# Kernel tuning notes

Hardware: AMD Instinct MI355X
Metric: run time of the kernel (lower is better)

The kernel has to match this reference:

```python
import jax, jax.numpy as jnp
import numpy as np

N_USER, N_ITEM, N_ENT = 60000, 30000, 15000
E_UI, E_IE = 1_000_000, 300_000
DIM, FACTOR_K, DIM_K, ITERS = 50, 2, 25, 4
INDEX = [(0, 1), (1, 0)] + [(1, j) for j in range(2, 8)]
I_LIST = [[0], [1, 2, 3, 4, 5, 6, 7]]


def _l2n(x):
    # F.normalize(p=2, dim=2), eps=1e-12
    return x / jnp.clip(jnp.linalg.norm(x, axis=2, keepdims=True), 1e-12)


def _forward(edges, embs_in, Wtk, at, W, q_rela):
    n_types = len(embs_in)
    # fac(): project each node type into factor_k subspaces [k, n, dim_k]
    embs = [_l2n(jax.nn.leaky_relu(jnp.einsum('nd,kde->kne', embs_in[i], Wtk[i]), 0.2))
            for i in range(n_types)]
    rows = [embs[a].shape[1] for (a, b) in INDEX]
    # r_rela init: uniform over factors, never fed back (as in the source)
    r_node = [jnp.full((FACTOR_K, rows[e]), 1.0 / FACTOR_K, dtype=embs[0].dtype)
              for e in range(len(INDEX))]

    def rela_update(edge, new_emb, old_emb, a, r_n, n_rows, q_r):
        u, col = edge[0], edge[1]
        # edge gather + attention score per factor: [k, E]
        ui = jnp.concatenate([new_emb[:, u], old_emb[:, col]], axis=2)  # [k,E,2*dk]
        e_ts_k = jax.nn.relu(jnp.einsum('ked,kd->ke', ui, a))
        vals = jnp.sum(e_ts_k * r_n[:, u], axis=0)  # [E]
        # sparse row-wise softmax (torch.sparse.softmax dim=1)
        m = jax.ops.segment_max(vals, u, num_segments=n_rows)
        ex = jnp.exp(vals - m[u])
        attn = ex / jax.ops.segment_sum(ex, u, num_segments=n_rows)[u]
        # sparse mm per factor: scatter attn-weighted neighbor features
        msg = attn[None, :, None] * old_emb[:, col]  # [k,E,dk]
        z = jax.vmap(lambda mk: jax.ops.segment_sum(mk, u, num_segments=n_rows))(msg)
        z = jnp.einsum('kne,ef->knf', jax.nn.leaky_relu(z, 0.2), W)
        r = jax.nn.softmax(jnp.einsum('kne,e->kn', jnp.tanh(z), q_r), axis=0)
        return r, z

    # note: in the source all_new_emb aliases all_ego_emb (same list), so updates persist
    for _ in range(ITERS):
        rl, el = [], []
        for e in range(len(INDEX)):
            a_i, b_i = INDEX[e]
            r, z = rela_update(edges[e], embs[a_i], embs[b_i], at[e], r_node[e], rows[e], q_rela[e])
            rl.append(r)
            el.append(z)
        for i in range(2):
            ego = embs[i]
            for j in I_LIST[i]:
                ego = ego + el[j] * rl[j][:, :, None]
            embs[i] = _l2n(ego)

    def flat(e):  # torch.cat(list(e), dim=1): [k,n,d] -> [n, k*d]
        k, n, d = e.shape
        return jnp.transpose(e, (1, 0, 2)).reshape(n, k * d)

    return jnp.concatenate([flat(embs[0]), flat(embs[1])], axis=0)


def setup_inputs() -> dict:
    key = jax.random.key(0)
    ks = jax.random.split(key, 40)
    inp = {}

    def edges(k1, k2, E, nr, nc):
        r = jax.random.randint(k1, (E,), 0, nr)
        c = jax.random.randint(k2, (E,), 0, nc)
        return jnp.stack([r, c]).astype(jnp.int32)

    inp['edge0'] = edges(ks[0], ks[1], E_UI, N_USER, N_ITEM)
    inp['edge1'] = edges(ks[2], ks[3], E_UI, N_ITEM, N_USER)
    for e in range(2, 8):
        inp[f'edge{e}'] = edges(ks[2 * e], ks[2 * e + 1], E_IE, N_ITEM, N_ENT)
    sizes = [N_USER, N_ITEM] + [N_ENT] * 6
    for i, n in enumerate(sizes):
        inp[f'emb{i}'] = jax.random.normal(ks[16 + i], (n, DIM), jnp.float32) * 0.1
    inp['Wtk'] = jax.random.normal(ks[30], (8, FACTOR_K, DIM, DIM_K), jnp.float32) * (2.0 / (DIM + DIM_K)) ** 0.5
    inp['at'] = jax.random.normal(ks[31], (8, FACTOR_K, 2 * DIM_K), jnp.float32) * 0.1
    inp['W'] = jax.random.normal(ks[32], (DIM_K, DIM_K), jnp.float32) * 0.2
    inp['q_rela'] = jax.random.normal(ks[33], (8, DIM_K), jnp.float32) * 0.2
    return inp


def reference(edge0, edge1, edge2, edge3, edge4, edge5, edge6, edge7,
              emb0, emb1, emb2, emb3, emb4, emb5, emb6, emb7,
              Wtk, at, W, q_rela):
    edges = [edge0, edge1, edge2, edge3, edge4, edge5, edge6, edge7]
    embs_in = [emb0, emb1, emb2, emb3, emb4, emb5, emb6, emb7]
    return _forward(edges, embs_in, Wtk, at, W, q_rela)
```

## Files before the change

### kernel.cpp

```cpp
#include <hip/hip_runtime.h>
#include <math.h>


#define KF 2
#define DK 25
#define DD 50
#define PS 52
#define ITERS 4
#define WPB 4

static __device__ __forceinline__ float leakyf(float x) { return x > 0.f ? x : 0.2f * x; }

static __device__ __forceinline__ float2 score_row50(const float* p, const float* a) {
    float s0 = 0.f, s1 = 0.f;
    #pragma unroll
    for (int f = 0; f < DK; ++f) {
        s0 = fmaf(p[f],      a[f],      s0);
        s1 = fmaf(p[DK + f], a[50 + f], s1);
    }
    return make_float2(s0, s1);
}
static __device__ __forceinline__ float2 score_col50(const float* p, const float* a) {
    float s0 = 0.f, s1 = 0.f;
    #pragma unroll
    for (int f = 0; f < DK; ++f) {
        s0 = fmaf(p[f],      a[25 + f], s0);
        s1 = fmaf(p[DK + f], a[75 + f], s1);
    }
    return make_float2(s0, s1);
}

struct FacArgs { const float* emb[8]; float* P[8]; const float* Wtk; int base[9]; };

__global__ void fac_kernel(FacArgs A) {
    int g = blockIdx.x * blockDim.x + threadIdx.x;
    if (g >= A.base[8]) return;
    int ty = 0;
    while (g >= A.base[ty + 1]) ++ty;
    int node = g - A.base[ty];
    const float* er = A.emb[ty] + (size_t)node * DD;
    const float* Wt = A.Wtk + (size_t)ty * KF * DD * DK;
    float x[DD];
    #pragma unroll
    for (int d = 0; d < DD; ++d) x[d] = er[d];
    float out[DD];
    #pragma unroll
    for (int k = 0; k < KF; ++k) {
        const float* Wk = Wt + k * DD * DK;
        float nrm = 0.f;
        for (int f = 0; f < DK; ++f) {
            float acc = 0.f;
            for (int d = 0; d < DD; ++d) acc = fmaf(x[d], Wk[d * DK + f], acc);
            acc = leakyf(acc);
            out[k * DK + f] = acc;
            nrm = fmaf(acc, acc, nrm);
        }
        float inv = 1.f / fmaxf(sqrtf(nrm), 1e-12f);
        for (int f = 0; f < DK; ++f) out[k * DK + f] *= inv;
    }
    float* Pr = A.P[ty] + (size_t)node * PS;
    #pragma unroll
    for (int j = 0; j < DD; ++j) Pr[j] = out[j];
    Pr[50] = 0.f; Pr[51] = 0.f;
}

struct EdgeArgs {
    const int* rows[8]; const int* cols[8];
    int* cnt;
    unsigned short* colind;
    int ebase[9];
    int rowbase[8];
};

__global__ void hist_kernel(EdgeArgs A) {
    int g = blockIdx.x * blockDim.x + threadIdx.x;
    if (g >= A.ebase[8]) return;
    int rel = 0;
    while (g >= A.ebase[rel + 1]) ++rel;
    int e = g - A.ebase[rel];
    atomicAdd(&A.cnt[A.rowbase[rel] + A.rows[rel][e]], 1);
}

__global__ __launch_bounds__(1024) void scan_part_kernel(int* a, int n, int* bsum) {
    __shared__ int lds[1024];
    int tid = threadIdx.x;
    int i = blockIdx.x * 1024 + tid;
    int v = (i < n) ? a[i] : 0;
    lds[tid] = v;
    __syncthreads();
    int x = v;
    for (int off = 1; off < 1024; off <<= 1) {
        int y = (tid >= off) ? lds[tid - off] : 0;
        __syncthreads();
        x += y;
        lds[tid] = x;
        __syncthreads();
    }
    if (i < n) a[i] = x - v;
    if (tid == 1023) bsum[blockIdx.x] = x;
}

__global__ __launch_bounds__(1024) void scan_bsum_kernel(int* bsum, int nb) {
    __shared__ int lds[1024];
    int tid = threadIdx.x;
    int v = (tid < nb) ? bsum[tid] : 0;
    lds[tid] = v;
    __syncthreads();
    int x = v;
    for (int off = 1; off < 1024; off <<= 1) {
        int y = (tid >= off) ? lds[tid - off] : 0;
        __syncthreads();
        x += y;
        lds[tid] = x;
        __syncthreads();
    }
    if (tid < nb) bsum[tid] = x - v;
}

__global__ __launch_bounds__(1024) void add_off_kernel(int* a, int n, const int* bsum) {
    int i = blockIdx.x * 1024 + threadIdx.x;
    if (i < n) a[i] += bsum[blockIdx.x];
}

__global__ void scatter_kernel(EdgeArgs A) {
    int g = blockIdx.x * blockDim.x + threadIdx.x;
    if (g >= A.ebase[8]) return;
    int rel = 0;
    while (g >= A.ebase[rel + 1]) ++rel;
    int e = g - A.ebase[rel];
    int p = atomicAdd(&A.cnt[A.rowbase[rel] + A.rows[rel][e]], 1);
    A.colind[p] = (unsigned short)A.cols[rel][e];
}

struct SbArgs { const float* Pb[6]; const float* at[6]; float2* sb[6]; int base[7]; };

__global__ void sb_kernel(SbArgs A) {
    int g = blockIdx.x * blockDim.x + threadIdx.x;
    if (g >= A.base[6]) return;
    int rel = 0;
    while (g >= A.base[rel + 1]) ++rel;
    int c = g - A.base[rel];
    const float* p = A.Pb[rel] + (size_t)c * PS;
    A.sb[rel][c] = score_col50(p, A.at[rel]);
}

struct ScoreArgs {
    const float* P0; const float* P1;
    const float* at;
    float2* sa[8]; float2* sb0; float2* sb1;
    int n0, n1;
};

__global__ void score01_kernel(ScoreArgs A) {
    int g = blockIdx.x * blockDim.x + threadIdx.x;
    if (g >= A.n0 + A.n1) return;
    if (g < A.n0) {
        const float* p = A.P0 + (size_t)g * PS;
        float pr[DD];
        #pragma unroll
        for (int j = 0; j < DD; ++j) pr[j] = p[j];
        A.sa[0][g] = score_row50(pr, A.at + 0);
        A.sb1[g]   = score_col50(pr, A.at + 100);
    } else {
        int node = g - A.n0;
        const float* p = A.P1 + (size_t)node * PS;
        float pr[DD];
        #pragma unroll
        for (int j = 0; j < DD; ++j) pr[j] = p[j];
        #pragma unroll
        for (int e = 1; e < 8; ++e) A.sa[e][node] = score_row50(pr, A.at + e * 100);
        A.sb0[node] = score_col50(pr, A.at + 0);
    }
}

struct PhaseArgs {
    const int* rowptr;
    const unsigned short* colind;
    const float* Pb[8];
    const float* q[8];
    const float2* sa[8]; const float2* sb[8];
    float* z[8]; float* r[8];
    const float* W;
    int rowbase[9];
};

__global__ __launch_bounds__(WPB * 64) void phase_kernel(PhaseArgs A, int totalRows) {
    int wave = blockIdx.x * WPB + (threadIdx.x >> 6);
    int lane = threadIdx.x & 63;
    if (wave >= totalRows) return;
    int rel = 0;
    while (wave >= A.rowbase[rel + 1]) ++rel;
    int u = wave - A.rowbase[rel];

    const unsigned short* colind = A.colind;
    const float* Pb = A.Pb[rel];
    const float* qv = A.q[rel];
    const float2* sb = A.sb[rel];
    float2 h = A.sa[rel][u];
    int beg = wave ? A.rowptr[wave - 1] : 0;
    int end = A.rowptr[wave];

    bool act = lane < DD;
    int grp4 = lane >> 4, sub4 = lane & 15;
    float ssum = 0.f;
    float4 a4 = make_float4(0.f, 0.f, 0.f, 0.f);

    for (int base = beg; base < end; base += 64) {
        int idx = base + lane;
        bool vld = idx < end;
        int cb = vld ? (int)colind[idx] : 0;
        float evl = 0.f;
        if (vld) {
            float2 sc = sb[cb];
            evl = __expf(0.5f * (fmaxf(h.x + sc.x, 0.f) + fmaxf(h.y + sc.y, 0.f)));
        }
        ssum += evl;
        int nb = min(64, end - base);
        #pragma unroll 2
        for (int t = 0; t < nb; t += 4) {
            int srcl = t + grp4;
            int c = __shfl(cb, srcl);
            float ev = __shfl(evl, srcl);
            const float4* pc = (const float4*)(Pb + (size_t)c * PS);
            float4 v = pc[sub4];
            a4.x = fmaf(ev, v.x, a4.x);
            a4.y = fmaf(ev, v.y, a4.y);
            a4.z = fmaf(ev, v.z, a4.z);
            a4.w = fmaf(ev, v.w, a4.w);
        }
    }
    #pragma unroll
    for (int off = 32; off >= 16; off >>= 1) {
        a4.x += __shfl_xor(a4.x, off);
        a4.y += __shfl_xor(a4.y, off);
        a4.z += __shfl_xor(a4.z, off);
        a4.w += __shfl_xor(a4.w, off);
    }
    #pragma unroll
    for (int off = 32; off; off >>= 1) ssum += __shfl_xor(ssum, off);

    int src = lane >> 2;
    float fx = __shfl(a4.x, src), fy = __shfl(a4.y, src);
    float fz = __shfl(a4.z, src), fw = __shfl(a4.w, src);
    float za = (lane & 1) ? ((lane & 2) ? fw : fy) : ((lane & 2) ? fz : fx);

    float inv = (ssum > 0.f) ? (1.f / ssum) : 0.f;
    float zl = act ? leakyf(za * inv) : 0.f;

    int fcol = act ? ((lane < DK) ? lane : (lane - DK)) : 0;
    int kbase = (act && lane >= DK) ? DK : 0;
    float o = 0.f;
    const float* W = A.W;
    #pragma unroll
    for (int d = 0; d < DK; ++d) {
        float zd = __shfl(zl, kbase + d);
        o = fmaf(zd, W[d * DK + fcol], o);
    }
    float th = act ? tanhf(o) * qv[fcol] : 0.f;
    float t0 = (lane < DK) ? th : 0.f;
    float t1 = th - t0;
    #pragma unroll
    for (int off = 32; off; off >>= 1) { t0 += __shfl_xor(t0, off); t1 += __shfl_xor(t1, off); }
    float m = fmaxf(t0, t1);
    float e0 = __expf(t0 - m), e1 = __expf(t1 - m);
    float rinv = 1.f / (e0 + e1);

    if (act) A.z[rel][(size_t)u * DD + lane] = o;
    if (lane == 0) {
        A.r[rel][(size_t)u * 2 + 0] = e0 * rinv;
        A.r[rel][(size_t)u * 2 + 1] = e1 * rinv;
    }
}

static __device__ __forceinline__ void l2norm_store(float* dst, const float* acc) {
    #pragma unroll
    for (int k = 0; k < KF; ++k) {
        float nrm = 0.f;
        for (int f = 0; f < DK; ++f) nrm = fmaf(acc[k * DK + f], acc[k * DK + f], nrm);
        float inv = 1.f / fmaxf(sqrtf(nrm), 1e-12f);
        for (int f = 0; f < DK; ++f) dst[k * DK + f] = acc[k * DK + f] * inv;
    }
}

struct EgoArgs { float* P0; float* P1; const float* zz[8]; const float* rr[8]; int n0, n1; };

__global__ void ego_kernel(EgoArgs A) {
    int g = blockIdx.x * blockDim.x + threadIdx.x;
    if (g >= A.n0 + A.n1) return;
    float acc[DD];
    if (g < A.n0) {
        float* Pr = A.P0 + (size_t)g * PS;
        const float* zr = A.zz[0] + (size_t)g * DD;
        float r0 = A.rr[0][(size_t)g * 2], r1 = A.rr[0][(size_t)g * 2 + 1];
        #pragma unroll
        for (int j = 0; j < DD; ++j) acc[j] = fmaf(zr[j], (j < DK ? r0 : r1), Pr[j]);
        l2norm_store(Pr, acc);
    } else {
        int node = g - A.n0;
        float* Pr = A.P1 + (size_t)node * PS;
        #pragma unroll
        for (int j = 0; j < DD; ++j) acc[j] = Pr[j];
        for (int e = 1; e < 8; ++e) {
            const float* zr = A.zz[e] + (size_t)node * DD;
            float r0 = A.rr[e][(size_t)node * 2], r1 = A.rr[e][(size_t)node * 2 + 1];
            #pragma unroll
            for (int j = 0; j < DD; ++j) acc[j] = fmaf(zr[j], (j < DK ? r0 : r1), acc[j]);
        }
        l2norm_store(Pr, acc);
    }
}

__global__ void out_kernel(const float* __restrict__ P0, const float* __restrict__ P1,
                           int n0, int n1, float* __restrict__ out) {
    int g = blockIdx.x * blockDim.x + threadIdx.x;
    if (g >= n0 + n1) return;
    const float* src = (g < n0) ? (P0 + (size_t)g * PS) : (P1 + (size_t)(g - n0) * PS);
    float* dst = out + (size_t)g * DD;
    #pragma unroll
    for (int j = 0; j < DD; ++j) dst[j] = src[j];
}

static inline int cdiv(int a, int b) { return (a + b - 1) / b; }

extern "C" void kernel_launch(void* const* d_in, const int* in_sizes, int n_in,
                              void* d_out, int out_size, void* d_ws, size_t ws_size,
                              hipStream_t stream) {
    const int* edge[8];
    int E[8];
    for (int e = 0; e < 8; ++e) { edge[e] = (const int*)d_in[e]; E[e] = in_sizes[e] / 2; }
    const float* emb[8];
    int nn[8];
    for (int i = 0; i < 8; ++i) { emb[i] = (const float*)d_in[8 + i]; nn[i] = in_sizes[8 + i] / DD; }
    const float* Wtk = (const float*)d_in[16];
    const float* at  = (const float*)d_in[17];
    const float* W   = (const float*)d_in[18];
    const float* q   = (const float*)d_in[19];
    float* out = (float*)d_out;

    static const int aIdx[8] = {0, 1, 1, 1, 1, 1, 1, 1};
    static const int bIdx[8] = {1, 0, 2, 3, 4, 5, 6, 7};
    int rows[8], ncol[8];
    for (int e = 0; e < 8; ++e) { rows[e] = nn[aIdx[e]]; ncol[e] = nn[bIdx[e]]; }
    int rowbase[9];
    rowbase[0] = 0;
    for (int e = 0; e < 8; ++e) rowbase[e + 1] = rowbase[e] + rows[e];
    int totalRows = rowbase[8];
    int ebase[9];
    ebase[0] = 0;
    for (int e = 0; e < 8; ++e) ebase[e + 1] = ebase[e] + E[e];
    int totE = ebase[8];

    char* w = (char*)d_ws;
    size_t off = 0;
    auto alloc_f  = [&](size_t n) { float*  p = (float*)(w + off);  off += n * 4; return p; };
    auto alloc_f2 = [&](size_t n) { float2* p = (float2*)(w + off); off += n * 8; return p; };
    auto alloc_i  = [&](size_t n) { int*    p = (int*)(w + off);    off += n * 4; return p; };
    float* P[8]; for (int i = 0; i < 8; ++i) P[i] = alloc_f((size_t)nn[i] * PS);
    float* z[8]; for (int e = 0; e < 8; ++e) z[e] = alloc_f((size_t)rows[e] * DD);
    float* r[8]; for (int e = 0; e < 8; ++e) r[e] = alloc_f((size_t)rows[e] * 2);
    float2* sb[8]; for (int e = 0; e < 8; ++e) sb[e] = alloc_f2((size_t)ncol[e]);
    float2* sa[8]; for (int e = 0; e < 8; ++e) sa[e] = alloc_f2((size_t)rows[e]);
    int* cnt = alloc_i((size_t)totalRows);
    int nchunks = cdiv(totalRows, 1024);
    int* bsum = alloc_i((size_t)nchunks);
    unsigned short* colind = (unsigned short*)(w + off);
    off += (size_t)totE * 2;
    (void)ws_size;

    const int B = 256;

    hipMemsetAsync(cnt, 0, (size_t)totalRows * 4, stream);
    EdgeArgs EA;
    for (int e = 0; e < 8; ++e) {
        EA.rows[e] = edge[e]; EA.cols[e] = edge[e] + E[e];
        EA.rowbase[e] = rowbase[e];
        EA.ebase[e] = ebase[e];
    }
    EA.ebase[8] = ebase[8];
    EA.cnt = cnt; EA.colind = colind;
    hist_kernel<<<cdiv(totE, B), B, 0, stream>>>(EA);
    scan_part_kernel<<<nchunks, 1024, 0, stream>>>(cnt, totalRows, bsum);
    scan_bsum_kernel<<<1, 1024, 0, stream>>>(bsum, nchunks);
    add_off_kernel<<<nchunks, 1024, 0, stream>>>(cnt, totalRows, bsum);
    scatter_kernel<<<cdiv(totE, B), B, 0, stream>>>(EA);

    FacArgs FA;
    FA.base[0] = 0;
    for (int i = 0; i < 8; ++i) { FA.emb[i] = emb[i]; FA.P[i] = P[i]; FA.base[i + 1] = FA.base[i] + nn[i]; }
    FA.Wtk = Wtk;
    fac_kernel<<<cdiv(FA.base[8], B), B, 0, stream>>>(FA);

    SbArgs SBs;
    SBs.base[0] = 0;
    for (int e = 2; e < 8; ++e) {
        SBs.Pb[e - 2] = P[bIdx[e]];
        SBs.at[e - 2] = at + (size_t)e * KF * DD;
        SBs.sb[e - 2] = sb[e];
        SBs.base[e - 1] = SBs.base[e - 2] + ncol[e];
    }
    sb_kernel<<<cdiv(SBs.base[6], B), B, 0, stream>>>(SBs);

    ScoreArgs SC;
    SC.P0 = P[0]; SC.P1 = P[1]; SC.at = at;
    for (int e = 0; e < 8; ++e) SC.sa[e] = sa[e];
    SC.sb0 = sb[0]; SC.sb1 = sb[1];
    SC.n0 = nn[0]; SC.n1 = nn[1];
    score01_kernel<<<cdiv(nn[0] + nn[1], B), B, 0, stream>>>(SC);

    PhaseArgs PA;
    PA.rowptr = cnt; PA.colind = colind;
    for (int e = 0; e < 8; ++e) {
        PA.Pb[e] = P[bIdx[e]];
        PA.q[e]  = q + (size_t)e * DK;
        PA.sa[e] = sa[e]; PA.sb[e] = sb[e];
        PA.z[e] = z[e]; PA.r[e] = r[e];
        PA.rowbase[e] = rowbase[e];
    }
    PA.rowbase[8] = rowbase[8];
    PA.W = W;
    EgoArgs GA;
    GA.P0 = P[0]; GA.P1 = P[1]; GA.n0 = nn[0]; GA.n1 = nn[1];
    for (int e = 0; e < 8; ++e) { GA.zz[e] = z[e]; GA.rr[e] = r[e]; }

    for (int it = 0; it < ITERS; ++it) {
        phase_kernel<<<cdiv(totalRows, WPB), WPB * 64, 0, stream>>>(PA, totalRows);
        ego_kernel<<<cdiv(nn[0] + nn[1], B), B, 0, stream>>>(GA);
        score01_kernel<<<cdiv(nn[0] + nn[1], B), B, 0, stream>>>(SC);
    }

    out_kernel<<<cdiv(nn[0] + nn[1], B), B, 0, stream>>>(P[0], P[1], nn[0], nn[1], out);
}
```

Baseline: 1.749 ms.

## Remap phase blocks per XCD, pad z rows, fuse output copy into ego kernel

Measured after the change: 1.940 ms. 10.9% more time.

```diff
diff --git a/kernel.cpp b/kernel.cpp
--- a/kernel.cpp
+++ b/kernel.cpp
@@ -185,7 +185,11 @@
 };
 
 __global__ __launch_bounds__(WPB * 64) void phase_kernel(PhaseArgs A, int totalRows) {
-    int wave = blockIdx.x * WPB + (threadIdx.x >> 6);
+    int nblk = gridDim.x;
+    int b = blockIdx.x;
+    int q8 = nblk >> 3, r8 = nblk & 7, xcd = b & 7, i8 = b >> 3;
+    int lb = xcd * q8 + min(xcd, r8) + i8;
+    int wave = lb * WPB + (threadIdx.x >> 6);
     int lane = threadIdx.x & 63;
     if (wave >= totalRows) return;
     int rel = 0;
@@ -202,6 +206,7 @@
 
     bool act = lane < DD;
     int grp4 = lane >> 4, sub4 = lane & 15;
+    bool ld = sub4 < 13;
     float ssum = 0.f;
     float4 a4 = make_float4(0.f, 0.f, 0.f, 0.f);
 
@@ -221,12 +226,14 @@
             int srcl = t + grp4;
             int c = __shfl(cb, srcl);
             float ev = __shfl(evl, srcl);
-            const float4* pc = (const float4*)(Pb + (size_t)c * PS);
-            float4 v = pc[sub4];
-            a4.x = fmaf(ev, v.x, a4.x);
-            a4.y = fmaf(ev, v.y, a4.y);
-            a4.z = fmaf(ev, v.z, a4.z);
-            a4.w = fmaf(ev, v.w, a4.w);
+            if (ld) {
+                const float4* pc = (const float4*)(Pb + (size_t)c * PS);
+                float4 v = pc[sub4];
+                a4.x = fmaf(ev, v.x, a4.x);
+                a4.y = fmaf(ev, v.y, a4.y);
+                a4.z = fmaf(ev, v.z, a4.z);
+                a4.w = fmaf(ev, v.w, a4.w);
+            }
         }
     }
     #pragma unroll
@@ -265,59 +272,69 @@
     float e0 = __expf(t0 - m), e1 = __expf(t1 - m);
     float rinv = 1.f / (e0 + e1);
 
-    if (act) A.z[rel][(size_t)u * DD + lane] = o;
+    if (act) A.z[rel][(size_t)u * PS + lane] = o;
     if (lane == 0) {
         A.r[rel][(size_t)u * 2 + 0] = e0 * rinv;
         A.r[rel][(size_t)u * 2 + 1] = e1 * rinv;
     }
 }
 
-static __device__ __forceinline__ void l2norm_store(float* dst, const float* acc) {
+struct EgoArgs {
+    float* P0; float* P1;
+    const float* zz[8];
+    const float* rr[8];
+    float* outp;
+    int n0, n1;
+};
+
+__global__ void ego_kernel(EgoArgs A) {
+    int g = blockIdx.x * blockDim.x + threadIdx.x;
+    if (g >= A.n0 + A.n1) return;
+    float acc[DD];
+    bool is0 = g < A.n0;
+    int node = is0 ? g : g - A.n0;
+    float* Pr = (is0 ? A.P0 : A.P1) + (size_t)node * PS;
+    {
+        const float4* p4 = (const float4*)Pr;
+        #pragma unroll
+        for (int t = 0; t < 12; ++t) {
+            float4 v = p4[t];
+            acc[4 * t] = v.x; acc[4 * t + 1] = v.y; acc[4 * t + 2] = v.z; acc[4 * t + 3] = v.w;
+        }
+        acc[48] = Pr[48]; acc[49] = Pr[49];
+    }
+    int jbeg = is0 ? 0 : 1, jend = is0 ? 1 : 8;
+    for (int j = jbeg; j < jend; ++j) {
+        const float* zr = A.zz[j] + (size_t)node * PS;
+        float r0 = A.rr[j][(size_t)node * 2], r1 = A.rr[j][(size_t)node * 2 + 1];
+        const float4* z4 = (const float4*)zr;
+        #pragma unroll
+        for (int t = 0; t < 12; ++t) {
+            float4 v = z4[t];
+            acc[4 * t]     = fmaf(v.x, (4 * t     < DK) ? r0 : r1, acc[4 * t]);
+            acc[4 * t + 1] = fmaf(v.y, (4 * t + 1 < DK) ? r0 : r1, acc[4 * t + 1]);
+            acc[4 * t + 2] = fmaf(v.z, (4 * t + 2 < DK) ? r0 : r1, acc[4 * t + 2]);
+            acc[4 * t + 3] = fmaf(v.w, (4 * t + 3 < DK) ? r0 : r1, acc[4 * t + 3]);
+        }
+        acc[48] = fmaf(zr[48], r1, acc[48]);
+        acc[49] = fmaf(zr[49], r1, acc[49]);
+    }
     #pragma unroll
     for (int k = 0; k < KF; ++k) {
         float nrm = 0.f;
+        #pragma unroll
         for (int f = 0; f < DK; ++f) nrm = fmaf(acc[k * DK + f], acc[k * DK + f], nrm);
         float inv = 1.f / fmaxf(sqrtf(nrm), 1e-12f);
-        for (int f = 0; f < DK; ++f) dst[k * DK + f] = acc[k * DK + f] * inv;
-    }
-}
-
-struct EgoArgs { float* P0; float* P1; const float* zz[8]; const float* rr[8]; int n0, n1; };
-
-__global__ void ego_kernel(EgoArgs A) {
-    int g = blockIdx.x * blockDim.x + threadIdx.x;
-    if (g >= A.n0 + A.n1) return;
-    float acc[DD];
-    if (g < A.n0) {
-        float* Pr = A.P0 + (size_t)g * PS;
-        const float* zr = A.zz[0] + (size_t)g * DD;
-        float r0 = A.rr[0][(size_t)g * 2], r1 = A.rr[0][(size_t)g * 2 + 1];
-        #pragma unroll
-        for (int j = 0; j < DD; ++j) acc[j] = fmaf(zr[j], (j < DK ? r0 : r1), Pr[j]);
-        l2norm_store(Pr, acc);
-    } else {
-        int node = g - A.n0;
-        float* Pr = A.P1 + (size_t)node * PS;
-        #pragma unroll
-        for (int j = 0; j < DD; ++j) acc[j] = Pr[j];
-        for (int e = 1; e < 8; ++e) {
-            const float* zr = A.zz[e] + (size_t)node * DD;
-            float r0 = A.rr[e][(size_t)node * 2], r1 = A.rr[e][(size_t)node * 2 + 1];
-            #pragma unroll
-            for (int j = 0; j < DD; ++j) acc[j] = fmaf(zr[j], (j < DK ? r0 : r1), acc[j]);
-        }
-        l2norm_store(Pr, acc);
-    }
-}
-
-__global__ void out_kernel(const float* __restrict__ P0, const float* __restrict__ P1,
-                           int n0, int n1, float* __restrict__ out) {
-    int g = blockIdx.x * blockDim.x + threadIdx.x;
-    if (g >= n0 + n1) return;
-    const float* src = (g < n0) ? (P0 + (size_t)g * PS) : (P1 + (size_t)(g - n0) * PS);
-    float* dst = out + (size_t)g * DD;
-    #pragma unroll
-    for (int j = 0; j < DD; ++j) dst[j] = src[j];
+        #pragma unroll
+        for (int f = 0; f < DK; ++f) acc[k * DK + f] *= inv;
+    }
+    #pragma unroll
+    for (int f = 0; f < DD; ++f) Pr[f] = acc[f];
+    if (A.outp) {
+        float* dst = A.outp + (size_t)g * DD;
+        #pragma unroll
+        for (int f = 0; f < DD; ++f) dst[f] = acc[f];
+    }
 }
 
 static inline int cdiv(int a, int b) { return (a + b - 1) / b; }
@@ -356,7 +373,7 @@
     auto alloc_f2 = [&](size_t n) { float2* p = (float2*)(w + off); off += n * 8; return p; };
     auto alloc_i  = [&](size_t n) { int*    p = (int*)(w + off);    off += n * 4; return p; };
     float* P[8]; for (int i = 0; i < 8; ++i) P[i] = alloc_f((size_t)nn[i] * PS);
-    float* z[8]; for (int e = 0; e < 8; ++e) z[e] = alloc_f((size_t)rows[e] * DD);
+    float* z[8]; for (int e = 0; e < 8; ++e) z[e] = alloc_f((size_t)rows[e] * PS);
     float* r[8]; for (int e = 0; e < 8; ++e) r[e] = alloc_f((size_t)rows[e] * 2);
     float2* sb[8]; for (int e = 0; e < 8; ++e) sb[e] = alloc_f2((size_t)ncol[e]);
     float2* sa[8]; for (int e = 0; e < 8; ++e) sa[e] = alloc_f2((size_t)rows[e]);
@@ -421,12 +438,13 @@
     EgoArgs GA;
     GA.P0 = P[0]; GA.P1 = P[1]; GA.n0 = nn[0]; GA.n1 = nn[1];
     for (int e = 0; e < 8; ++e) { GA.zz[e] = z[e]; GA.rr[e] = r[e]; }
+    GA.outp = nullptr;
 
     for (int it = 0; it < ITERS; ++it) {
         phase_kernel<<<cdiv(totalRows, WPB), WPB * 64, 0, stream>>>(PA, totalRows);
+        GA.outp = (it == ITERS - 1) ? out : nullptr;
         ego_kernel<<<cdiv(nn[0] + nn[1], B), B, 0, stream>>>(GA);
-        score01_kernel<<<cdiv(nn[0] + nn[1], B), B, 0, stream>>>(SC);
-    }
-
-    out_kernel<<<cdiv(nn[0] + nn[1], B), B, 0, stream>>>(P[0], P[1], nn[0], nn[1], out);
-}
+        if (it != ITERS - 1)
+            score01_kernel<<<cdiv(nn[0] + nn[1], B), B, 0, stream>>>(SC);
+    }
+}
```
